# Performance work log

Hardware: AMD Instinct MI355X
Metric: run time of the kernel (lower is better)

The kernel has to match this reference:

```python
import jax, jax.numpy as jnp
import numpy as np

N = 8192      # number of tree nodes
IN = 1024     # in_dim
M = 1024      # effective mem_dim = 2 * mem_dim_init
K = 8         # max children (complete 8-ary tree)


def _linear_init(key, out_dim, in_dim):
    k1, k2 = jax.random.split(key)
    s = 1.0 / np.sqrt(in_dim)
    w = jax.random.uniform(k1, (out_dim, in_dim), minval=-s, maxval=s, dtype=jnp.float32)
    b = jax.random.uniform(k2, (out_dim,), minval=-s, maxval=s, dtype=jnp.float32)
    return w, b


def setup_inputs() -> dict:
    key = jax.random.key(0)
    ks = jax.random.split(key, 5)
    w_ioux, b_ioux = _linear_init(ks[0], 3 * M, IN)
    w_iouh, b_iouh = _linear_init(ks[1], 3 * M, M)
    w_fx, b_fx = _linear_init(ks[2], M, IN)
    w_fh, b_fh = _linear_init(ks[3], M, M)
    inputs = jax.random.normal(ks[4], (N, IN), dtype=jnp.float32)
    # Complete K-ary tree: children of node p are p*K+1 .. p*K+K (clipped).
    # Pad with index N, which addresses an always-zero dummy row.
    ch = np.full((N, K), N, dtype=np.int32)
    for j in range(K):
        idx = np.arange(N) * K + 1 + j
        valid = idx < N
        ch[valid, j] = idx[valid]
    return dict(inputs=inputs, children=jnp.asarray(ch),
                w_ioux=w_ioux, b_ioux=b_ioux, w_iouh=w_iouh, b_iouh=b_iouh,
                w_fx=w_fx, b_fx=b_fx, w_fh=w_fh, b_fh=b_fh)


def reference(inputs, children, w_ioux, b_ioux, w_iouh, b_iouh, w_fx, b_fx, w_fh, b_fh):
    # Precompute the input-side projections for all nodes at once.
    iou_x = inputs @ w_ioux.T + b_ioux   # [N, 3M]
    fx_x = inputs @ w_fx.T + b_fx        # [N, M]
    h0 = jnp.zeros((N + 1, M), inputs.dtype)  # row N is the zero pad slot
    c0 = jnp.zeros((N + 1, M), inputs.dtype)

    def step(carry, t):
        h_buf, c_buf = carry
        ch = children[t]           # [K] child indices (pad = N -> zero rows)
        ch_h = h_buf[ch]           # [K, M] real child h's
        ch_c = c_buf[ch]           # [K, M] real child c's
        # Faithful to original: for internal nodes child_c/child_h are SWAPPED,
        # so the 'child_h_sum' and f-gate inputs use the real c's, while the
        # forgotten memory (fc) multiplies the real h's. Leaves: all zeros.
        csum = ch_c.sum(0)                                   # [M]
        iou = iou_x[t] + csum @ w_iouh.T + b_iouh            # [3M]
        i_g, o_g, u_g = jnp.split(iou, 3)
        i_g = jax.nn.sigmoid(i_g)
        o_g = jax.nn.sigmoid(o_g)
        u_g = jnp.tanh(u_g)
        f = jax.nn.sigmoid(ch_c @ w_fh.T + b_fh + fx_x[t])   # [K, M]
        c = i_g * u_g + (f * ch_h).sum(0)                    # [M]
        h = o_g * jnp.tanh(c)
        return (h_buf.at[t].set(h), c_buf.at[t].set(c)), None

    # Children always have larger indices than their parent, so processing
    # t = N-1 .. 0 matches the original reverse-BFS (leaves-first) order.
    order = jnp.arange(N - 1, -1, -1)
    (h_buf, c_buf), _ = jax.lax.scan(step, (h0, c0), order)
    root_h = h_buf[0][None, :]   # [1, M]
    root_c = c_buf[0][None, :]   # [1, M]
    return root_h, root_c
```

## Files before the change

### kernel.cpp

```cpp
#include <hip/hip_runtime.h>

typedef __bf16 bf16x8 __attribute__((ext_vector_type(8)));
typedef __attribute__((ext_vector_type(4))) float f4;

#define AS1 __attribute__((address_space(1)))
#define AS3 __attribute__((address_space(3)))

__device__ __forceinline__ unsigned short f2bf(float f) {
    union { float f; unsigned int u; } x; x.f = f;
    return (unsigned short)((x.u + 0x7fffu + ((x.u >> 16) & 1u)) >> 16);
}
__device__ __forceinline__ float bf2f(unsigned short u) {
    union { unsigned int u; float f; } x; x.u = (unsigned int)u << 16;
    return x.f;
}
__device__ __forceinline__ float fsigm(float x) {
    return __builtin_amdgcn_rcpf(1.f + __expf(-x));
}
__device__ __forceinline__ float ftanh(float x) {
    return 1.f - 2.f * __builtin_amdgcn_rcpf(1.f + __expf(2.f * x));
}
__device__ __forceinline__ void gload_lds16(const unsigned short* g, unsigned short* l) {
    __builtin_amdgcn_global_load_lds((const AS1 unsigned int*)g, (AS3 unsigned int*)l, 16, 0, 0);
}
__device__ __forceinline__ void bar() {
    asm volatile("" ::: "memory");
    __builtin_amdgcn_s_barrier();
    asm volatile("" ::: "memory");
}

__global__ void prep_all_k(const float* __restrict__ inputs, const float* __restrict__ w_ioux,
                           const float* __restrict__ w_fx, const float* __restrict__ w_iouh,
                           const float* __restrict__ w_fh,
                           const float* __restrict__ b_ioux, const float* __restrict__ b_iouh,
                           const float* __restrict__ b_fx, const float* __restrict__ b_fh,
                           unsigned short* __restrict__ Xbf, unsigned short* __restrict__ Wiouxbf,
                           unsigned short* __restrict__ Wfxbf, unsigned short* __restrict__ Whbf,
                           unsigned short* __restrict__ Wfhbf,
                           float* __restrict__ bias_iou, float* __restrict__ bias_f,
                           unsigned short* __restrict__ c_bf, unsigned short* __restrict__ h_bf) {
    int b = blockIdx.x;
    if (b < 16384) {
        int idx = b * 256 + threadIdx.x;
        const float* src; unsigned short* dst; int rel;
        if (idx < 2097152)      { src = inputs; dst = Xbf;     rel = idx; }
        else if (idx < 2883584) { src = w_ioux; dst = Wiouxbf; rel = idx - 2097152; }
        else if (idx < 3145728) { src = w_fx;   dst = Wfxbf;   rel = idx - 2883584; }
        else if (idx < 3932160) { src = w_iouh; dst = Whbf;    rel = idx - 3145728; }
        else                    { src = w_fh;   dst = Wfhbf;   rel = idx - 3932160; }
        float4 v = reinterpret_cast<const float4*>(src)[rel];
        ushort4 o; o.x = f2bf(v.x); o.y = f2bf(v.y); o.z = f2bf(v.z); o.w = f2bf(v.w);
        reinterpret_cast<ushort4*>(dst)[rel] = o;
    } else if (b < 16400) {
        int idx = (b - 16384) * 256 + threadIdx.x;
        if (idx < 3072) bias_iou[idx] = b_ioux[idx] + b_iouh[idx];
        else { int j = idx - 3072; bias_f[j] = b_fx[j] + b_fh[j]; }
    } else {
        int j = (b - 16400) * 256 + threadIdx.x;
        size_t o = (size_t)8192 * 1024 + j;
        c_bf[o] = 0; h_bf[o] = 0;
    }
}

__device__ __forceinline__ void stage_half(const unsigned short* __restrict__ G, int M,
                                           int trow0, int kt, unsigned short* lds_region, int tid) {
#pragma unroll
    for (int ii = 0; ii < 2; ++ii) {
        int c = ii * 512 + tid;
        int r = c >> 3, sl = c & 7;
        int row = min(trow0 + r, M - 1);
        gload_lds16(G + (size_t)row * 1024 + kt * 64 + ((sl ^ (r & 7)) * 8),
                    lds_region + c * 8);
    }
}
__device__ __forceinline__ bf16x8 rdfrag(const unsigned short* region, int rowih, int kslot) {
    return *reinterpret_cast<const bf16x8*>(&region[rowih * 64 + ((kslot ^ (rowih & 7)) * 8)]);
}

#define RD_A(AF, REG, FB)                                                        \
    _Pragma("unroll") for (int f_ = 0; f_ < 4; ++f_)                             \
    _Pragma("unroll") for (int s_ = 0; s_ < 2; ++s_)                             \
        (AF)[f_][s_] = rdfrag((REG), ((FB) + f_) * 16 + fr, s_ * 4 + q);
#define RD_B(BQ, REG, GB)                                                        \
    _Pragma("unroll") for (int g_ = 0; g_ < 2; ++g_)                             \
    _Pragma("unroll") for (int s_ = 0; s_ < 2; ++s_)                             \
        (BQ)[g_][s_] = rdfrag((REG), bcol0 + ((GB) + g_) * 16 + fr, s_ * 4 + q);
#define MF16(FB, GB, AF, BQ)                                                     \
    __builtin_amdgcn_s_setprio(1);                                               \
    _Pragma("unroll") for (int s_ = 0; s_ < 2; ++s_)                             \
    _Pragma("unroll") for (int f_ = 0; f_ < 4; ++f_)                             \
    _Pragma("unroll") for (int g_ = 0; g_ < 2; ++g_)                             \
        acc[(FB) + f_][(GB) + g_] = __builtin_amdgcn_mfma_f32_16x16x32_bf16(     \
            (AF)[f_][s_], (BQ)[g_][s_], acc[(FB) + f_][(GB) + g_], 0, 0, 0);     \
    __builtin_amdgcn_s_setprio(0);

__device__ __forceinline__ void gemm256_core(const unsigned short* __restrict__ Am,
                                             const unsigned short* __restrict__ Bm,
                                             int M, int tm, int tn,
                                             unsigned short* ls, f4 acc[8][4]) {
    const int tid = threadIdx.x;
    const int l = tid & 63, w = tid >> 6;
    const int wm = w >> 2, wn = w & 3;
    const int fr = l & 15, q = l >> 4;
    const int bcol0 = (wn & 1) * 64;
    const int BIGM = 1 << 30;

    unsigned short* S0 = ls;
    unsigned short* S1 = ls + 32768;
    const unsigned short* Ar0 = S0 + wm * 8192;
    const unsigned short* Br0 = S0 + (2 + (wn >> 1)) * 8192;
    const unsigned short* Ar1 = S1 + wm * 8192;
    const unsigned short* Br1 = S1 + (2 + (wn >> 1)) * 8192;

#pragma unroll
    for (int i = 0; i < 8; ++i)
#pragma unroll
        for (int j = 0; j < 4; ++j) acc[i][j] = (f4){0.f, 0.f, 0.f, 0.f};

    stage_half(Am, M, tm,       0, S0 + 0 * 8192, tid);
    stage_half(Am, M, tm + 128, 0, S0 + 1 * 8192, tid);
    stage_half(Bm, BIGM, tn,       0, S0 + 2 * 8192, tid);
    stage_half(Bm, BIGM, tn + 128, 0, S0 + 3 * 8192, tid);
    stage_half(Bm, BIGM, tn,       1, S1 + 2 * 8192, tid);
    stage_half(Bm, BIGM, tn + 128, 1, S1 + 3 * 8192, tid);
    asm volatile("s_waitcnt vmcnt(4)" ::: "memory");
    bar();

    for (int i = 0; i < 8; ++i) {
        bf16x8 afA[4][2], afB[4][2], bq01[2][2], bq23[2][2];
        RD_A(afA, Ar0, 0)
        RD_B(bq01, Br0, 0)
        stage_half(Am, M, tm,       2 * i + 1, S1 + 0 * 8192, tid);
        bar();
        MF16(0, 0, afA, bq01)
        bar();
        RD_B(bq23, Br0, 2)
        stage_half(Am, M, tm + 128, 2 * i + 1, S1 + 1 * 8192, tid);
        bar();
        MF16(0, 2, afA, bq23)
        bar();
        RD_A(afB, Ar0, 4)
        if (i < 7) stage_half(Bm, BIGM, tn,       2 * i + 2, S0 + 2 * 8192, tid);
        bar();
        MF16(4, 2, afB, bq23)
        bar();
        if (i < 7) {
            stage_half(Bm, BIGM, tn + 128, 2 * i + 2, S0 + 3 * 8192, tid);
            asm volatile("s_waitcnt vmcnt(4)" ::: "memory");
        } else {
            asm volatile("s_waitcnt vmcnt(0)" ::: "memory");
        }
        bar();
        MF16(4, 0, afB, bq01)
        bar();
        RD_A(afA, Ar1, 0)
        RD_B(bq01, Br1, 0)
        if (i < 7) stage_half(Am, M, tm,       2 * i + 2, S0 + 0 * 8192, tid);
        bar();
        MF16(0, 0, afA, bq01)
        bar();
        RD_B(bq23, Br1, 2)
        if (i < 7) stage_half(Am, M, tm + 128, 2 * i + 2, S0 + 1 * 8192, tid);
        bar();
        MF16(0, 2, afA, bq23)
        bar();
        RD_A(afB, Ar1, 4)
        if (i < 7) stage_half(Bm, BIGM, tn,       2 * i + 3, S1 + 2 * 8192, tid);
        bar();
        MF16(4, 2, afB, bq23)
        bar();
        if (i < 7) {
            stage_half(Bm, BIGM, tn + 128, 2 * i + 3, S1 + 3 * 8192, tid);
            asm volatile("s_waitcnt vmcnt(4)" ::: "memory");
        } else {
            asm volatile("s_waitcnt vmcnt(0)" ::: "memory");
        }
        bar();
        MF16(4, 0, afB, bq01)
        bar();
    }
}

__global__ __launch_bounds__(512, 2)
void gemm_big_k(const unsigned short* __restrict__ Xbf, const unsigned short* __restrict__ Wioux,
                const unsigned short* __restrict__ Wfx,
                const float* __restrict__ bias_iou, const float* __restrict__ bias_f,
                unsigned short* __restrict__ P_iou, unsigned short* __restrict__ P_f) {
    __shared__ unsigned short ls[65536];
    int b = blockIdx.x;
    b = (b & 7) * 50 + (b >> 3);
    const unsigned short* Bm; unsigned short* Cp; const float* biasp;
    int tm, tn, ldc;
    if (b < 384) {
        int st = b / 24, wt = b % 24;
        tm = ((st >> 2) * 8 + wt / 3) * 256;
        tn = ((st & 3) * 3 + wt % 3) * 256;
        Bm = Wioux; Cp = P_iou; biasp = bias_iou; ldc = 3072;
    } else {
        int bb = b - 384;
        tm = (bb & 3) * 256; tn = (bb >> 2) * 256;
        Bm = Wfx; Cp = P_f; biasp = bias_f; ldc = 1024;
    }
    f4 acc[8][4];
    gemm256_core(Xbf, Bm, 8192, tm, tn, ls, acc);

    const int l = threadIdx.x & 63, w = threadIdx.x >> 6;
    const int wm = w >> 2, wn = w & 3;
    const int fr = l & 15, q = l >> 4;
#pragma unroll
    for (int f = 0; f < 8; ++f)
#pragma unroll
        for (int g = 0; g < 4; ++g) {
            int col = tn + wn * 64 + g * 16 + fr;
            float bv = biasp[col];
#pragma unroll
            for (int r = 0; r < 4; ++r) {
                int row = tm + wm * 128 + f * 16 + q * 4 + r;
                Cp[(size_t)row * ldc + col] = f2bf(acc[f][g][r] + bv);
            }
        }
}

__device__ __forceinline__ void gemm_core_db(const unsigned short* __restrict__ A,
                                             const unsigned short* __restrict__ B,
                                             int M, int tile_m, int tile_n, int kb, int nsteps,
                                             unsigned short* lsA, unsigned short* lsB,
                                             f4 acc[4][4]) {
    const int K = 1024;
    const int tid = threadIdx.x;
    const int l = tid & 63, wid = tid >> 6;
    const int wm = wid >> 1, wn = wid & 1;
    const int fr = l & 15, q = l >> 4;

#pragma unroll
    for (int i = 0; i < 4; ++i)
#pragma unroll
        for (int j = 0; j < 4; ++j) acc[i][j] = (f4){0.f, 0.f, 0.f, 0.f};

    const unsigned short* ga[4]; const unsigned short* gb[4];
    unsigned short *la[4], *lb[4];
#pragma unroll
    for (int i = 0; i < 4; ++i) {
        int chunk = i * 256 + tid;
        int row = chunk >> 3, slot = chunk & 7;
        int scol = (slot ^ (row & 7)) * 8;
        ga[i] = A + (size_t)min(tile_m + row, M - 1) * K + kb * 64 + scol;
        gb[i] = B + (size_t)(tile_n + row) * K + kb * 64 + scol;
        la[i] = lsA + chunk * 8;
        lb[i] = lsB + chunk * 8;
    }
#pragma unroll
    for (int i = 0; i < 4; ++i) gload_lds16(ga[i], la[i]);
#pragma unroll
    for (int i = 0; i < 4; ++i) gload_lds16(gb[i], lb[i]);

    int roffA[4], roffB[4];
#pragma unroll
    for (int f = 0; f < 4; ++f) {
        roffA[f] = (wm * 64 + f * 16 + fr) * 64;
        roffB[f] = (wn * 64 + f * 16 + fr) * 64;
    }
    const int sw = fr & 7;
    int cur = 0;
    for (int t = 0; t < nsteps; ++t) {
        if (t < nsteps - 1) {
            int k0 = (t + 1) * 64;
            int nb = (cur ^ 1) * 8192;
#pragma unroll
            for (int i = 0; i < 4; ++i) gload_lds16(ga[i] + k0, la[i] + nb);
#pragma unroll
            for (int i = 0; i < 4; ++i) gload_lds16(gb[i] + k0, lb[i] + nb);
            asm volatile("s_waitcnt vmcnt(8)" ::: "memory");
        } else {
            asm volatile("s_waitcnt vmcnt(0)" ::: "memory");
        }
        __builtin_amdgcn_s_barrier();
        const unsigned short* bA = lsA + cur * 8192;
        const unsigned short* bB = lsB + cur * 8192;
        bf16x8 af[4][2], bq[4][2];
#pragma unroll
        for (int f = 0; f < 4; ++f)
#pragma unroll
            for (int s = 0; s < 2; ++s) {
                int sl = ((s * 4 + q) ^ sw) * 8;
                af[f][s] = *reinterpret_cast<const bf16x8*>(&bA[roffA[f] + sl]);
                bq[f][s] = *reinterpret_cast<const bf16x8*>(&bB[roffB[f] + sl]);
            }
#pragma unroll
        for (int s = 0; s < 2; ++s)
#pragma unroll
            for (int i = 0; i < 4; ++i)
#pragma unroll
                for (int j = 0; j < 4; ++j)
                    acc[i][j] = __builtin_amdgcn_mfma_f32_16x16x32_bf16(af[i][s], bq[j][s], acc[i][j], 0, 0, 0);
        __builtin_amdgcn_s_barrier();
        cur ^= 1;
    }
}

__global__ void leafact_csum_k(const unsigned short* __restrict__ P_iou,
                               unsigned short* __restrict__ h_bf, unsigned short* __restrict__ c_bf,
                               unsigned short* __restrict__ csum_bf) {
    int b = blockIdx.x;
    int j = threadIdx.x * 4;
    if (b < 896) {
        int p = 128 + b;
        float s0 = 0.f, s1 = 0.f, s2 = 0.f, s3 = 0.f;
#pragma unroll
        for (int k = 0; k < 8; ++k) {
            int t = p * 8 + 1 + k;
            const unsigned short* pp = P_iou + (size_t)t * 3072 + j;
            ushort4 pi = *reinterpret_cast<const ushort4*>(pp);
            ushort4 po = *reinterpret_cast<const ushort4*>(pp + 1024);
            ushort4 pu = *reinterpret_cast<const ushort4*>(pp + 2048);
            float c0 = fsigm(bf2f(pi.x)) * ftanh(bf2f(pu.x));
            float c1 = fsigm(bf2f(pi.y)) * ftanh(bf2f(pu.y));
            float c2 = fsigm(bf2f(pi.z)) * ftanh(bf2f(pu.z));
            float c3 = fsigm(bf2f(pi.w)) * ftanh(bf2f(pu.w));
            ushort4 cb, hb;
            cb.x = f2bf(c0); hb.x = f2bf(fsigm(bf2f(po.x)) * ftanh(c0));
            cb.y = f2bf(c1); hb.y = f2bf(fsigm(bf2f(po.y)) * ftanh(c1));
            cb.z = f2bf(c2); hb.z = f2bf(fsigm(bf2f(po.z)) * ftanh(c2));
            cb.w = f2bf(c3); hb.w = f2bf(fsigm(bf2f(po.w)) * ftanh(c3));
            size_t o = (size_t)t * 1024 + j;
            *reinterpret_cast<ushort4*>(c_bf + o) = cb;
            *reinterpret_cast<ushort4*>(h_bf + o) = hb;
            s0 += c0; s1 += c1; s2 += c2; s3 += c3;
        }
        ushort4 sv; sv.x = f2bf(s0); sv.y = f2bf(s1); sv.z = f2bf(s2); sv.w = f2bf(s3);
        *reinterpret_cast<ushort4*>(csum_bf + (size_t)p * 1024 + j) = sv;
    } else {
        const int t = 1024;
        const unsigned short* pp = P_iou + (size_t)t * 3072 + j;
        ushort4 pi = *reinterpret_cast<const ushort4*>(pp);
        ushort4 po = *reinterpret_cast<const ushort4*>(pp + 1024);
        ushort4 pu = *reinterpret_cast<const ushort4*>(pp + 2048);
        float c0 = fsigm(bf2f(pi.x)) * ftanh(bf2f(pu.x));
        float c1 = fsigm(bf2f(pi.y)) * ftanh(bf2f(pu.y));
        float c2 = fsigm(bf2f(pi.z)) * ftanh(bf2f(pu.z));
        float c3 = fsigm(bf2f(pi.w)) * ftanh(bf2f(pu.w));
        ushort4 cb, hb;
        cb.x = f2bf(c0); hb.x = f2bf(fsigm(bf2f(po.x)) * ftanh(c0));
        cb.y = f2bf(c1); hb.y = f2bf(fsigm(bf2f(po.y)) * ftanh(c1));
        cb.z = f2bf(c2); hb.z = f2bf(fsigm(bf2f(po.z)) * ftanh(c2));
        cb.w = f2bf(c3); hb.w = f2bf(fsigm(bf2f(po.w)) * ftanh(c3));
        size_t o = (size_t)t * 1024 + j;
        *reinterpret_cast<ushort4*>(c_bf + o) = cb;
        *reinterpret_cast<ushort4*>(h_bf + o) = hb;
    }
}

__device__ __forceinline__ void csum_dev(const unsigned short* __restrict__ c_bf,
                                         unsigned short* __restrict__ csum_bf, int lo, int w) {
    int tt = w >> 8, j = (w & 255) * 4;
    int t = lo + tt;
    size_t base = (size_t)(t * 8 + 1) * 1024 + j;
    float s0 = 0.f, s1 = 0.f, s2 = 0.f, s3 = 0.f;
#pragma unroll
    for (int k = 0; k < 8; ++k) {
        ushort4 v = *reinterpret_cast<const ushort4*>(c_bf + base + (size_t)k * 1024);
        s0 += bf2f(v.x); s1 += bf2f(v.y); s2 += bf2f(v.z); s3 += bf2f(v.w);
    }
    ushort4 o; o.x = f2bf(s0); o.y = f2bf(s1); o.z = f2bf(s2); o.w = f2bf(s3);
    *reinterpret_cast<ushort4*>(csum_bf + (size_t)t * 1024 + j) = o;
}

__global__ void csum_k(const unsigned short* __restrict__ c_bf, unsigned short* __restrict__ csum_bf,
                       int lo, int n) {
    int w = blockIdx.x * blockDim.x + threadIdx.x;
    if (w < n * 256) csum_dev(c_bf, csum_bf, lo, w);
}

__global__ void node_update_k(const unsigned short* __restrict__ P_iou,
                              const unsigned short* __restrict__ P_f,
                              const float* __restrict__ out_iouh, const float* __restrict__ out_f,
                              unsigned short* __restrict__ h_bf, unsigned short* __restrict__ c_bf,
                              float* __restrict__ out, int lo, int n) {
    int w = blockIdx.x * blockDim.x + threadIdx.x;
    if (w >= n * 256) return;
    int tt = w >> 8, j = (w & 255) * 4;
    int t = lo + tt;
    const unsigned short* p = P_iou + (size_t)t * 3072 + j;
    ushort4 pi4 = *reinterpret_cast<const ushort4*>(p);
    ushort4 po4 = *reinterpret_cast<const ushort4*>(p + 1024);
    ushort4 pu4 = *reinterpret_cast<const ushort4*>(p + 2048);
    const float* oi = out_iouh + (size_t)tt * 3072 + j;
    f4 oii = *reinterpret_cast<const f4*>(oi);
    f4 oio = *reinterpret_cast<const f4*>(oi + 1024);
    f4 oiu = *reinterpret_cast<const f4*>(oi + 2048);
    ushort4 pf4 = *reinterpret_cast<const ushort4*>(P_f + (size_t)t * 1024 + j);
    float pf[4] = {bf2f(pf4.x), bf2f(pf4.y), bf2f(pf4.z), bf2f(pf4.w)};
    float a[4], og[4];
    a[0] = fsigm(bf2f(pi4.x) + oii[0]) * ftanh(bf2f(pu4.x) + oiu[0]);
    a[1] = fsigm(bf2f(pi4.y) + oii[1]) * ftanh(bf2f(pu4.y) + oiu[1]);
    a[2] = fsigm(bf2f(pi4.z) + oii[2]) * ftanh(bf2f(pu4.z) + oiu[2]);
    a[3] = fsigm(bf2f(pi4.w) + oii[3]) * ftanh(bf2f(pu4.w) + oiu[3]);
    og[0] = fsigm(bf2f(po4.x) + oio[0]);
    og[1] = fsigm(bf2f(po4.y) + oio[1]);
    og[2] = fsigm(bf2f(po4.z) + oio[2]);
    og[3] = fsigm(bf2f(po4.w) + oio[3]);
#pragma unroll
    for (int k = 0; k < 8; ++k) {
        f4 fo = *reinterpret_cast<const f4*>(out_f + (size_t)(tt * 8 + k) * 1024 + j);
        ushort4 hc = *reinterpret_cast<const ushort4*>(h_bf + (size_t)(t * 8 + 1 + k) * 1024 + j);
        a[0] += fsigm(pf[0] + fo[0]) * bf2f(hc.x);
        a[1] += fsigm(pf[1] + fo[1]) * bf2f(hc.y);
        a[2] += fsigm(pf[2] + fo[2]) * bf2f(hc.z);
        a[3] += fsigm(pf[3] + fo[3]) * bf2f(hc.w);
    }
    float h0 = og[0] * ftanh(a[0]);
    float h1 = og[1] * ftanh(a[1]);
    float h2 = og[2] * ftanh(a[2]);
    float h3 = og[3] * ftanh(a[3]);
    size_t o = (size_t)t * 1024 + j;
    ushort4 cb; cb.x = f2bf(a[0]); cb.y = f2bf(a[1]); cb.z = f2bf(a[2]); cb.w = f2bf(a[3]);
    ushort4 hb; hb.x = f2bf(h0); hb.y = f2bf(h1); hb.z = f2bf(h2); hb.w = f2bf(h3);
    *reinterpret_cast<ushort4*>(c_bf + o) = cb;
    *reinterpret_cast<ushort4*>(h_bf + o) = hb;
    if (t == 0) {
        f4 hv = {h0, h1, h2, h3};
        f4 cv = {a[0], a[1], a[2], a[3]};
        *reinterpret_cast<f4*>(out + j) = hv;
        *reinterpret_cast<f4*>(out + 1024 + j) = cv;
    }
}

struct GDesc {
    const unsigned short* A;
    const unsigned short* B;
    float* C;
    int M;
    int ldc;
    int tiles_n;
    int tiles_total;
};

__global__ __launch_bounds__(256)
void gemm_dual_k(GDesc d0, GDesc d1) {
    __shared__ unsigned short lsA[16384];
    __shared__ unsigned short lsB[16384];
    int b = blockIdx.x;
    GDesc d; int bb;
    if (b < d0.tiles_total) { d = d0; bb = b; }
    else { d = d1; bb = b - d0.tiles_total; }
    const int tile_m = (bb / d.tiles_n) * 128;
    const int tile_n = (bb % d.tiles_n) * 128;
    f4 acc[4][4];
    gemm_core_db(d.A, d.B, d.M, tile_m, tile_n, 0, 16, lsA, lsB, acc);

    const int l = threadIdx.x & 63, wid = threadIdx.x >> 6;
    const int wm = wid >> 1, wn = wid & 1;
    const int fr = l & 15, q = l >> 4;
#pragma unroll
    for (int i = 0; i < 4; ++i)
#pragma unroll
        for (int j = 0; j < 4; ++j) {
            int col = tile_n + wn * 64 + fr + j * 16;
#pragma unroll
            for (int r = 0; r < 4; ++r) {
                int row = tile_m + wm * 64 + q * 4 + i * 16 + r;
                if (row < d.M) d.C[(size_t)row * d.ldc + col] = acc[i][j][r];
            }
        }
}

__global__ __launch_bounds__(256)
void gemm_tail_k(const unsigned short* __restrict__ csum_lvl,
                 const unsigned short* __restrict__ cchild,
                 const unsigned short* __restrict__ Whbf, const unsigned short* __restrict__ Wfhbf,
                 float* __restrict__ part_iouh, float* __restrict__ part_f, int n) {
    __shared__ unsigned short lsA[16384];
    __shared__ unsigned short lsB[16384];
    int b = blockIdx.x;
    const unsigned short* A; const unsigned short* Bw; float* C;
    int M, ldc, tm, tn, split;
    if (b < 96) {
        split = b & 3; int tile = b >> 2;
        A = csum_lvl; Bw = Whbf; M = n; ldc = 3072; tm = 0; tn = tile * 128;
        C = part_iouh + (size_t)split * 64 * 3072;
    } else {
        int bb = b - 96;
        split = bb & 3; int tile = bb >> 2;
        A = cchild; Bw = Wfhbf; M = 8 * n; ldc = 1024;
        tm = (tile >> 3) * 128; tn = (tile & 7) * 128;
        C = part_f + (size_t)split * 512 * 1024;
    }
    f4 acc[4][4];
    gemm_core_db(A, Bw, M, tm, tn, split * 4, 4, lsA, lsB, acc);

    const int l = threadIdx.x & 63, wid = threadIdx.x >> 6;
    const int wm = wid >> 1, wn = wid & 1;
    const int fr = l & 15, q = l >> 4;
#pragma unroll
    for (int i = 0; i < 4; ++i)
#pragma unroll
        for (int j = 0; j < 4; ++j) {
            int col = tn + wn * 64 + fr + j * 16;
#pragma unroll
            for (int r = 0; r < 4; ++r) {
                int row = tm + wm * 64 + q * 4 + i * 16 + r;
                if (row < M) C[(size_t)row * ldc + col] = acc[i][j][r];
            }
        }
}

__global__ void node_update_tail_k(const unsigned short* __restrict__ P_iou,
                                   const unsigned short* __restrict__ P_f,
                                   const float* __restrict__ part_iouh,
                                   const float* __restrict__ part_f,
                                   unsigned short* __restrict__ h_bf, unsigned short* __restrict__ c_bf,
                                   float* __restrict__ out, int lo, int n) {
    int w = blockIdx.x * blockDim.x + threadIdx.x;
    if (w >= n * 256) return;
    int tt = w >> 8, j = (w & 255) * 4;
    int t = lo + tt;
    f4 oii = {0.f, 0.f, 0.f, 0.f}, oio = oii, oiu = oii;
#pragma unroll
    for (int s = 0; s < 4; ++s) {
        const float* base = part_iouh + (size_t)s * 64 * 3072 + (size_t)tt * 3072 + j;
        oii += *reinterpret_cast<const f4*>(base);
        oio += *reinterpret_cast<const f4*>(base + 1024);
        oiu += *reinterpret_cast<const f4*>(base + 2048);
    }
    const unsigned short* p = P_iou + (size_t)t * 3072 + j;
    ushort4 pi4 = *reinterpret_cast<const ushort4*>(p);
    ushort4 po4 = *reinterpret_cast<const ushort4*>(p + 1024);
    ushort4 pu4 = *reinterpret_cast<const ushort4*>(p + 2048);
    ushort4 pf4 = *reinterpret_cast<const ushort4*>(P_f + (size_t)t * 1024 + j);
    float pf[4] = {bf2f(pf4.x), bf2f(pf4.y), bf2f(pf4.z), bf2f(pf4.w)};
    float a[4], og[4];
    a[0] = fsigm(bf2f(pi4.x) + oii[0]) * ftanh(bf2f(pu4.x) + oiu[0]);
    a[1] = fsigm(bf2f(pi4.y) + oii[1]) * ftanh(bf2f(pu4.y) + oiu[1]);
    a[2] = fsigm(bf2f(pi4.z) + oii[2]) * ftanh(bf2f(pu4.z) + oiu[2]);
    a[3] = fsigm(bf2f(pi4.w) + oii[3]) * ftanh(bf2f(pu4.w) + oiu[3]);
    og[0] = fsigm(bf2f(po4.x) + oio[0]);
    og[1] = fsigm(bf2f(po4.y) + oio[1]);
    og[2] = fsigm(bf2f(po4.z) + oio[2]);
    og[3] = fsigm(bf2f(po4.w) + oio[3]);
#pragma unroll
    for (int k = 0; k < 8; ++k) {
        f4 fo = {0.f, 0.f, 0.f, 0.f};
#pragma unroll
        for (int s = 0; s < 4; ++s)
            fo += *reinterpret_cast<const f4*>(part_f + (size_t)s * 512 * 1024 +
                                               (size_t)(tt * 8 + k) * 1024 + j);
        ushort4 hc = *reinterpret_cast<const ushort4*>(h_bf + (size_t)(t * 8 + 1 + k) * 1024 + j);
        a[0] += fsigm(pf[0] + fo[0]) * bf2f(hc.x);
        a[1] += fsigm(pf[1] + fo[1]) * bf2f(hc.y);
        a[2] += fsigm(pf[2] + fo[2]) * bf2f(hc.z);
        a[3] += fsigm(pf[3] + fo[3]) * bf2f(hc.w);
    }
    float h0 = og[0] * ftanh(a[0]);
    float h1 = og[1] * ftanh(a[1]);
    float h2 = og[2] * ftanh(a[2]);
    float h3 = og[3] * ftanh(a[3]);
    size_t o = (size_t)t * 1024 + j;
    ushort4 cb; cb.x = f2bf(a[0]); cb.y = f2bf(a[1]); cb.z = f2bf(a[2]); cb.w = f2bf(a[3]);
    ushort4 hb; hb.x = f2bf(h0); hb.y = f2bf(h1); hb.z = f2bf(h2); hb.w = f2bf(h3);
    *reinterpret_cast<ushort4*>(c_bf + o) = cb;
    *reinterpret_cast<ushort4*>(h_bf + o) = hb;
    if (t == 0) {
        f4 hv = {h0, h1, h2, h3};
        f4 cv = {a[0], a[1], a[2], a[3]};
        *reinterpret_cast<f4*>(out + j) = hv;
        *reinterpret_cast<f4*>(out + 1024 + j) = cv;
    }
}

extern "C" void kernel_launch(void* const* d_in, const int* in_sizes, int n_in,
                              void* d_out, int out_size, void* d_ws, size_t ws_size,
                              hipStream_t stream) {
    const float* inputs = (const float*)d_in[0];
    const float* w_ioux = (const float*)d_in[2];
    const float* b_ioux = (const float*)d_in[3];
    const float* w_iouh = (const float*)d_in[4];
    const float* b_iouh = (const float*)d_in[5];
    const float* w_fx   = (const float*)d_in[6];
    const float* b_fx   = (const float*)d_in[7];
    const float* w_fh   = (const float*)d_in[8];
    const float* b_fh   = (const float*)d_in[9];
    float* out = (float*)d_out;

    char* ws = (char*)d_ws;
    size_t off = 0;
    auto alloc = [&](size_t bytes) -> void* {
        void* p = ws + off;
        off += (bytes + 255) & ~(size_t)255;
        return p;
    };
    unsigned short* Xbf     = (unsigned short*)alloc((size_t)8192 * 1024 * 2);
    unsigned short* Wiouxbf = (unsigned short*)alloc((size_t)3072 * 1024 * 2);
    unsigned short* Wfxbf   = (unsigned short*)alloc((size_t)1024 * 1024 * 2);
    unsigned short* Whbf    = (unsigned short*)alloc((size_t)3072 * 1024 * 2);
    unsigned short* Wfhbf   = (unsigned short*)alloc((size_t)1024 * 1024 * 2);
    float* bias_iou         = (float*)alloc((size_t)3072 * 4);
    float* bias_f           = (float*)alloc((size_t)1024 * 4);
    unsigned short* P_iou   = (unsigned short*)alloc((size_t)8192 * 3072 * 2);
    unsigned short* P_f     = (unsigned short*)alloc((size_t)1024 * 1024 * 2);
    unsigned short* c_bf    = (unsigned short*)alloc((size_t)8193 * 1024 * 2);
    unsigned short* h_bf    = (unsigned short*)alloc((size_t)8193 * 1024 * 2);
    unsigned short* csum_bf = (unsigned short*)alloc((size_t)1024 * 1024 * 2);
    float* out_iouh         = (float*)alloc((size_t)512 * 3072 * 4);
    float* out_f            = (float*)alloc((size_t)4096 * 1024 * 4);
    float* part_iouh        = (float*)alloc((size_t)4 * 64 * 3072 * 4);
    float* part_f           = (float*)alloc((size_t)4 * 512 * 1024 * 4);

    prep_all_k<<<dim3(16404), dim3(256), 0, stream>>>(
        inputs, w_ioux, w_fx, w_iouh, w_fh, b_ioux, b_iouh, b_fx, b_fh,
        Xbf, Wiouxbf, Wfxbf, Whbf, Wfhbf, bias_iou, bias_f, c_bf, h_bf);

    gemm_big_k<<<dim3(400), dim3(512), 0, stream>>>(Xbf, Wiouxbf, Wfxbf,
                                                    bias_iou, bias_f, P_iou, P_f);
    leafact_csum_k<<<dim3(897), dim3(256), 0, stream>>>(P_iou, h_bf, c_bf, csum_bf);

    {
        const int lo = 585, n = 439;
        GDesc d0, d1;
        d0.A = csum_bf + (size_t)lo * 1024; d0.B = Whbf; d0.C = out_iouh;
        d0.M = n; d0.ldc = 3072; d0.tiles_n = 24;
        d0.tiles_total = ((n + 127) / 128) * 24;
        d1.A = c_bf + (size_t)(lo * 8 + 1) * 1024; d1.B = Wfhbf; d1.C = out_f;
        d1.M = 8 * n; d1.ldc = 1024; d1.tiles_n = 8;
        d1.tiles_total = ((8 * n + 127) / 128) * 8;
        gemm_dual_k<<<dim3(d0.tiles_total + d1.tiles_total), dim3(256), 0, stream>>>(d0, d1);
        node_update_k<<<dim3(n), dim3(256), 0, stream>>>(
            P_iou, P_f, out_iouh, out_f, h_bf, c_bf, out, lo, n);
    }
    {
        const int lo = 73, n = 512;
        csum_k<<<dim3(55), dim3(256), 0, stream>>>(c_bf, csum_bf, 73, 55);
        GDesc d0, d1;
        d0.A = csum_bf + (size_t)lo * 1024; d0.B = Whbf; d0.C = out_iouh;
        d0.M = n; d0.ldc = 3072; d0.tiles_n = 24;
        d0.tiles_total = ((n + 127) / 128) * 24;
        d1.A = c_bf + (size_t)(lo * 8 + 1) * 1024; d1.B = Wfhbf; d1.C = out_f;
        d1.M = 8 * n; d1.ldc = 1024; d1.tiles_n = 8;
        d1.tiles_total = ((8 * n + 127) / 128) * 8;
        gemm_dual_k<<<dim3(d0.tiles_total + d1.tiles_total), dim3(256), 0, stream>>>(d0, d1);
        node_update_k<<<dim3(n), dim3(256), 0, stream>>>(
            P_iou, P_f, out_iouh, out_f, h_bf, c_bf, out, lo, n);
    }
    const int T_LO[3] = {9, 1, 0};
    const int T_N[3]  = {64, 8, 1};
    for (int lv = 0; lv < 3; ++lv) {
        int lo = T_LO[lv], n = T_N[lv];
        csum_k<<<dim3(n), dim3(256), 0, stream>>>(c_bf, csum_bf, lo, n);
        int fm_tiles = (8 * n + 127) / 128;
        int nblk = 96 + fm_tiles * 8 * 4;
        gemm_tail_k<<<dim3(nblk), dim3(256), 0, stream>>>(
            csum_bf + (size_t)lo * 1024, c_bf + (size_t)(lo * 8 + 1) * 1024,
            Whbf, Wfhbf, part_iouh, part_f, n);
        node_update_tail_k<<<dim3(n), dim3(256), 0, stream>>>(
            P_iou, P_f, part_iouh, part_f, h_bf, c_bf, out, lo, n);
    }
    (void)in_sizes; (void)n_in; (void)out_size; (void)ws_size;
}
```

Measured before the change: 199.7 us.

## Fuse child c-sum into tail GEMM and drop row clamping in big GEMM

The per-level csum_k launch for the three top tree levels is removed. The iouh-branch blocks of gemm_tail_k now sum the eight children's c rows directly into a swizzled LDS A tile and run their own double-buffered MFMA loop over the weight slice. The big input-projection GEMM also drops its min() row clamp and adds an lgkmcnt wait before a barrier. This saves three kernel launches and the round trip through the csum buffer on the latency-bound tail, in exchange for redundant summation across the 24 column tiles and no out-of-bounds guard on the A rows.

New measurement: 197.4 us. No clear change (-1.2%).

```diff
diff --git a/kernel.cpp b/kernel.cpp
--- a/kernel.cpp
+++ b/kernel.cpp
@@ -62,14 +62,13 @@
     }
 }
 
-__device__ __forceinline__ void stage_half(const unsigned short* __restrict__ G, int M,
+__device__ __forceinline__ void stage_half(const unsigned short* __restrict__ G,
                                            int trow0, int kt, unsigned short* lds_region, int tid) {
 #pragma unroll
     for (int ii = 0; ii < 2; ++ii) {
         int c = ii * 512 + tid;
         int r = c >> 3, sl = c & 7;
-        int row = min(trow0 + r, M - 1);
-        gload_lds16(G + (size_t)row * 1024 + kt * 64 + ((sl ^ (r & 7)) * 8),
+        gload_lds16(G + (size_t)(trow0 + r) * 1024 + kt * 64 + ((sl ^ (r & 7)) * 8),
                     lds_region + c * 8);
     }
 }
@@ -96,14 +95,13 @@
 
 __device__ __forceinline__ void gemm256_core(const unsigned short* __restrict__ Am,
                                              const unsigned short* __restrict__ Bm,
-                                             int M, int tm, int tn,
+                                             int tm, int tn,
                                              unsigned short* ls, f4 acc[8][4]) {
     const int tid = threadIdx.x;
     const int l = tid & 63, w = tid >> 6;
     const int wm = w >> 2, wn = w & 3;
     const int fr = l & 15, q = l >> 4;
     const int bcol0 = (wn & 1) * 64;
-    const int BIGM = 1 << 30;
 
     unsigned short* S0 = ls;
     unsigned short* S1 = ls + 32768;
@@ -117,12 +115,12 @@
 #pragma unroll
         for (int j = 0; j < 4; ++j) acc[i][j] = (f4){0.f, 0.f, 0.f, 0.f};
 
-    stage_half(Am, M, tm,       0, S0 + 0 * 8192, tid);
-    stage_half(Am, M, tm + 128, 0, S0 + 1 * 8192, tid);
-    stage_half(Bm, BIGM, tn,       0, S0 + 2 * 8192, tid);
-    stage_half(Bm, BIGM, tn + 128, 0, S0 + 3 * 8192, tid);
-    stage_half(Bm, BIGM, tn,       1, S1 + 2 * 8192, tid);
-    stage_half(Bm, BIGM, tn + 128, 1, S1 + 3 * 8192, tid);
+    stage_half(Am, tm,       0, S0 + 0 * 8192, tid);
+    stage_half(Am, tm + 128, 0, S0 + 1 * 8192, tid);
+    stage_half(Bm, tn,       0, S0 + 2 * 8192, tid);
+    stage_half(Bm, tn + 128, 0, S0 + 3 * 8192, tid);
+    stage_half(Bm, tn,       1, S1 + 2 * 8192, tid);
+    stage_half(Bm, tn + 128, 1, S1 + 3 * 8192, tid);
     asm volatile("s_waitcnt vmcnt(4)" ::: "memory");
     bar();
 
@@ -130,22 +128,23 @@
         bf16x8 afA[4][2], afB[4][2], bq01[2][2], bq23[2][2];
         RD_A(afA, Ar0, 0)
         RD_B(bq01, Br0, 0)
-        stage_half(Am, M, tm,       2 * i + 1, S1 + 0 * 8192, tid);
+        stage_half(Am, tm,       2 * i + 1, S1 + 0 * 8192, tid);
+        asm volatile("s_waitcnt lgkmcnt(8)" ::: "memory");
         bar();
         MF16(0, 0, afA, bq01)
         bar();
         RD_B(bq23, Br0, 2)
-        stage_half(Am, M, tm + 128, 2 * i + 1, S1 + 1 * 8192, tid);
+        stage_half(Am, tm + 128, 2 * i + 1, S1 + 1 * 8192, tid);
         bar();
         MF16(0, 2, afA, bq23)
         bar();
         RD_A(afB, Ar0, 4)
-        if (i < 7) stage_half(Bm, BIGM, tn,       2 * i + 2, S0 + 2 * 8192, tid);
+        if (i < 7) stage_half(Bm, tn,       2 * i + 2, S0 + 2 * 8192, tid);
         bar();
         MF16(4, 2, afB, bq23)
         bar();
         if (i < 7) {
-            stage_half(Bm, BIGM, tn + 128, 2 * i + 2, S0 + 3 * 8192, tid);
+            stage_half(Bm, tn + 128, 2 * i + 2, S0 + 3 * 8192, tid);
             asm volatile("s_waitcnt vmcnt(4)" ::: "memory");
         } else {
             asm volatile("s_waitcnt vmcnt(0)" ::: "memory");
@@ -155,22 +154,23 @@
         bar();
         RD_A(afA, Ar1, 0)
         RD_B(bq01, Br1, 0)
-        if (i < 7) stage_half(Am, M, tm,       2 * i + 2, S0 + 0 * 8192, tid);
+        if (i < 7) stage_half(Am, tm,       2 * i + 2, S0 + 0 * 8192, tid);
+        asm volatile("s_waitcnt lgkmcnt(8)" ::: "memory");
         bar();
         MF16(0, 0, afA, bq01)
         bar();
         RD_B(bq23, Br1, 2)
-        if (i < 7) stage_half(Am, M, tm + 128, 2 * i + 2, S0 + 1 * 8192, tid);
+        if (i < 7) stage_half(Am, tm + 128, 2 * i + 2, S0 + 1 * 8192, tid);
         bar();
         MF16(0, 2, afA, bq23)
         bar();
         RD_A(afB, Ar1, 4)
-        if (i < 7) stage_half(Bm, BIGM, tn,       2 * i + 3, S1 + 2 * 8192, tid);
+        if (i < 7) stage_half(Bm, tn,       2 * i + 3, S1 + 2 * 8192, tid);
         bar();
         MF16(4, 2, afB, bq23)
         bar();
         if (i < 7) {
-            stage_half(Bm, BIGM, tn + 128, 2 * i + 3, S1 + 3 * 8192, tid);
+            stage_half(Bm, tn + 128, 2 * i + 3, S1 + 3 * 8192, tid);
             asm volatile("s_waitcnt vmcnt(4)" ::: "memory");
         } else {
             asm volatile("s_waitcnt vmcnt(0)" ::: "memory");
@@ -202,7 +202,7 @@
         Bm = Wfx; Cp = P_f; biasp = bias_f; ldc = 1024;
     }
     f4 acc[8][4];
-    gemm256_core(Xbf, Bm, 8192, tm, tn, ls, acc);
+    gemm256_core(Xbf, Bm, tm, tn, ls, acc);
 
     const int l = threadIdx.x & 63, w = threadIdx.x >> 6;
     const int wm = w >> 2, wn = w & 3;
@@ -350,8 +350,10 @@
     }
 }
 
-__device__ __forceinline__ void csum_dev(const unsigned short* __restrict__ c_bf,
-                                         unsigned short* __restrict__ csum_bf, int lo, int w) {
+__global__ void csum_k(const unsigned short* __restrict__ c_bf, unsigned short* __restrict__ csum_bf,
+                       int lo, int n) {
+    int w = blockIdx.x * blockDim.x + threadIdx.x;
+    if (w >= n * 256) return;
     int tt = w >> 8, j = (w & 255) * 4;
     int t = lo + tt;
     size_t base = (size_t)(t * 8 + 1) * 1024 + j;
@@ -363,12 +365,6 @@
     }
     ushort4 o; o.x = f2bf(s0); o.y = f2bf(s1); o.z = f2bf(s2); o.w = f2bf(s3);
     *reinterpret_cast<ushort4*>(csum_bf + (size_t)t * 1024 + j) = o;
-}
-
-__global__ void csum_k(const unsigned short* __restrict__ c_bf, unsigned short* __restrict__ csum_bf,
-                       int lo, int n) {
-    int w = blockIdx.x * blockDim.x + threadIdx.x;
-    if (w < n * 256) csum_dev(c_bf, csum_bf, lo, w);
 }
 
 __global__ void node_update_k(const unsigned short* __restrict__ P_iou,
@@ -465,32 +461,104 @@
 }
 
 __global__ __launch_bounds__(256)
-void gemm_tail_k(const unsigned short* __restrict__ csum_lvl,
-                 const unsigned short* __restrict__ cchild,
+void gemm_tail_k(const unsigned short* __restrict__ c_bf,
                  const unsigned short* __restrict__ Whbf, const unsigned short* __restrict__ Wfhbf,
-                 float* __restrict__ part_iouh, float* __restrict__ part_f, int n) {
+                 float* __restrict__ part_iouh, float* __restrict__ part_f, int lo, int n) {
     __shared__ unsigned short lsA[16384];
     __shared__ unsigned short lsB[16384];
+    const int tid = threadIdx.x;
+    const int l = tid & 63, wid = tid >> 6;
+    const int wm = wid >> 1, wn = wid & 1;
+    const int fr = l & 15, q = l >> 4;
     int b = blockIdx.x;
-    const unsigned short* A; const unsigned short* Bw; float* C;
-    int M, ldc, tm, tn, split;
+    f4 acc[4][4];
+    float* C; int M, ldc, tm, tn;
+
     if (b < 96) {
-        split = b & 3; int tile = b >> 2;
-        A = csum_lvl; Bw = Whbf; M = n; ldc = 3072; tm = 0; tn = tile * 128;
+        const int split = b & 3, tile = b >> 2;
+        M = n; ldc = 3072; tm = 0; tn = tile * 128;
         C = part_iouh + (size_t)split * 64 * 3072;
+        for (int e = tid; e < n * 64; e += 256) {
+            int r = e >> 6, c4 = e & 63;
+            size_t gbase = (size_t)((lo + r) * 8 + 1) * 1024 + split * 256 + c4 * 4;
+            float s0 = 0.f, s1 = 0.f, s2 = 0.f, s3 = 0.f;
+#pragma unroll
+            for (int k = 0; k < 8; ++k) {
+                ushort4 v = *reinterpret_cast<const ushort4*>(c_bf + gbase + (size_t)k * 1024);
+                s0 += bf2f(v.x); s1 += bf2f(v.y); s2 += bf2f(v.z); s3 += bf2f(v.w);
+            }
+            ushort4 o; o.x = f2bf(s0); o.y = f2bf(s1); o.z = f2bf(s2); o.w = f2bf(s3);
+            int sl8 = c4 >> 1, half = c4 & 1;
+            int phys = (sl8 & ~7) | ((sl8 & 7) ^ (r & 7));
+            *reinterpret_cast<ushort4*>(&lsA[r * 256 + phys * 8 + half * 4]) = o;
+        }
+        const unsigned short* gb[4]; unsigned short* lb[4];
+#pragma unroll
+        for (int i = 0; i < 4; ++i) {
+            int chunk = i * 256 + tid;
+            int row = chunk >> 3, slot = chunk & 7;
+            int scol = (slot ^ (row & 7)) * 8;
+            gb[i] = Whbf + (size_t)(tn + row) * 1024 + split * 256 + scol;
+            lb[i] = lsB + chunk * 8;
+        }
+#pragma unroll
+        for (int i = 0; i < 4; ++i) gload_lds16(gb[i], lb[i]);
+        asm volatile("s_waitcnt lgkmcnt(0)" ::: "memory");
+        __builtin_amdgcn_s_barrier();
+
+#pragma unroll
+        for (int i2 = 0; i2 < 4; ++i2)
+#pragma unroll
+            for (int j2 = 0; j2 < 4; ++j2) acc[i2][j2] = (f4){0.f, 0.f, 0.f, 0.f};
+        int roffB[4], rA[4];
+#pragma unroll
+        for (int f = 0; f < 4; ++f) {
+            roffB[f] = (wn * 64 + f * 16 + fr) * 64;
+            rA[f] = min(wm * 64 + f * 16 + fr, n - 1);
+        }
+        const int sw = fr & 7;
+        int cur = 0;
+        for (int t = 0; t < 4; ++t) {
+            if (t < 3) {
+                int nb = (cur ^ 1) * 8192;
+#pragma unroll
+                for (int i = 0; i < 4; ++i) gload_lds16(gb[i] + (t + 1) * 64, lb[i] + nb);
+                asm volatile("s_waitcnt vmcnt(4)" ::: "memory");
+            } else {
+                asm volatile("s_waitcnt vmcnt(0)" ::: "memory");
+            }
+            __builtin_amdgcn_s_barrier();
+            const unsigned short* bB = lsB + cur * 8192;
+            bf16x8 af[4][2], bq[4][2];
+#pragma unroll
+            for (int f = 0; f < 4; ++f)
+#pragma unroll
+                for (int s = 0; s < 2; ++s) {
+                    int x = s * 4 + q;
+                    af[f][s] = *reinterpret_cast<const bf16x8*>(
+                        &lsA[rA[f] * 256 + (t * 8 + (x ^ (rA[f] & 7))) * 8]);
+                    bq[f][s] = *reinterpret_cast<const bf16x8*>(&bB[roffB[f] + ((x ^ sw) * 8)]);
+                }
+#pragma unroll
+            for (int s = 0; s < 2; ++s)
+#pragma unroll
+                for (int i = 0; i < 4; ++i)
+#pragma unroll
+                    for (int j = 0; j < 4; ++j)
+                        acc[i][j] = __builtin_amdgcn_mfma_f32_16x16x32_bf16(af[i][s], bq[j][s], acc[i][j], 0, 0, 0);
+            __builtin_amdgcn_s_barrier();
+            cur ^= 1;
+        }
     } else {
         int bb = b - 96;
-        split = bb & 3; int tile = bb >> 2;
-        A = cchild; Bw = Wfhbf; M = 8 * n; ldc = 1024;
+        const int split = bb & 3, tile = bb >> 2;
+        M = 8 * n; ldc = 1024;
         tm = (tile >> 3) * 128; tn = (tile & 7) * 128;
         C = part_f + (size_t)split * 512 * 1024;
-    }
-    f4 acc[4][4];
-    gemm_core_db(A, Bw, M, tm, tn, split * 4, 4, lsA, lsB, acc);
-
-    const int l = threadIdx.x & 63, wid = threadIdx.x >> 6;
-    const int wm = wid >> 1, wn = wid & 1;
-    const int fr = l & 15, q = l >> 4;
+        gemm_core_db(c_bf + (size_t)(lo * 8 + 1) * 1024, Wfhbf, M, tm, tn, split * 4, 4,
+                     lsA, lsB, acc);
+    }
+
 #pragma unroll
     for (int i = 0; i < 4; ++i)
 #pragma unroll
@@ -644,12 +712,10 @@
     const int T_N[3]  = {64, 8, 1};
     for (int lv = 0; lv < 3; ++lv) {
         int lo = T_LO[lv], n = T_N[lv];
-        csum_k<<<dim3(n), dim3(256), 0, stream>>>(c_bf, csum_bf, lo, n);
         int fm_tiles = (8 * n + 127) / 128;
         int nblk = 96 + fm_tiles * 8 * 4;
         gemm_tail_k<<<dim3(nblk), dim3(256), 0, stream>>>(
-            csum_bf + (size_t)lo * 1024, c_bf + (size_t)(lo * 8 + 1) * 1024,
-            Whbf, Wfhbf, part_iouh, part_f, n);
+            c_bf, Whbf, Wfhbf, part_iouh, part_f, lo, n);
         node_update_tail_k<<<dim3(n), dim3(256), 0, stream>>>(
             P_iou, P_f, part_iouh, part_f, h_bf, c_bf, out, lo, n);
     }
```
